# Optimization experiments

Measured on AMD Instinct MI355X. Metric: run time of the kernel, lower is better.

## Reference

```python
import jax, jax.numpy as jnp
import numpy as np

N, E, G = 10000, 320000, 256
IN_NODE, OUT_NODE, IN_EDGE, HID = 32, 32, 16, 64
BN_EPS = 1e-5


def setup_inputs() -> dict:
    key = jax.random.key(0)
    ks = jax.random.split(key, 8)
    return {
        "x": jax.random.normal(ks[0], (N, IN_NODE), jnp.float32),
        "edge_attr": jax.random.normal(ks[1], (E, IN_EDGE), jnp.float32),
        "edge_index": jax.random.randint(ks[2], (2, E), 0, N),
        "batch": jnp.sort(jax.random.randint(ks[3], (N,), 0, G)),
        "W1": jax.random.normal(ks[4], (IN_EDGE, HID), jnp.float32) * 0.1,
        "b1": jnp.zeros((HID,), jnp.float32),
        "gamma": jnp.ones((HID,), jnp.float32),
        "beta": jnp.zeros((HID,), jnp.float32),
        "W2": jax.random.normal(ks[5], (HID, IN_NODE * OUT_NODE), jnp.float32) * 0.05,
        "b2": jnp.zeros((IN_NODE * OUT_NODE,), jnp.float32),
        "W_root": jax.random.normal(ks[6], (IN_NODE, OUT_NODE), jnp.float32) * 0.1,
        "bias": jnp.zeros((OUT_NODE,), jnp.float32),
        "num_graphs": G,
    }


def reference(x, edge_attr, edge_index, batch, W1, b1, gamma, beta, W2, b2, W_root, bias, num_graphs):
    src, dst = edge_index[0], edge_index[1]
    # edge MLP: Linear -> BatchNorm1d (training-mode batch stats) -> ReLU -> Linear
    h = edge_attr @ W1 + b1                                   # [E, HID]
    mu = jnp.mean(h, axis=0)
    var = jnp.var(h, axis=0)
    h = (h - mu) * jax.lax.rsqrt(var + BN_EPS) * gamma + beta
    h = jax.nn.relu(h)
    w_e = (h @ W2 + b2).reshape(-1, x.shape[1], W_root.shape[1])  # [E, in, out]
    # gather source features, per-edge matmul, scatter-add to targets
    msgs = jnp.einsum('ei,eio->eo', x[src], w_e)              # [E, out]
    aggr = jax.ops.segment_sum(msgs, dst, num_segments=x.shape[0])
    out = aggr + x @ W_root + bias                            # [N, out]
    # global mean pool per graph
    pooled = jax.ops.segment_sum(out, batch, num_segments=num_graphs)
    counts = jax.ops.segment_sum(jnp.ones((x.shape[0],), x.dtype), batch, num_segments=num_graphs)
    return pooled / jnp.maximum(counts, 1.0)[:, None]
```

## Files before the change

### kernel.cpp

```cpp
#include <hip/hip_runtime.h>
#include <stdint.h>

typedef unsigned short u16;
typedef _Float16 f16x2 __attribute__((ext_vector_type(2)));
union U32F16 { uint32_t u; f16x2 h; };

__device__ __forceinline__ float bf2f(u16 v) {
    union { uint32_t u; float f; } c; c.u = ((uint32_t)v) << 16; return c.f;
}
__device__ __forceinline__ u16 f2bf(float f) {
    union { uint32_t u; float f; } c; c.f = f;
    uint32_t u = c.u;
    return (u16)((u + 0x7FFF + ((u >> 16) & 1)) >> 16);
}
__device__ __forceinline__ float loadf(const void* p, size_t i, int isbf) {
    return isbf ? bf2f(((const u16*)p)[i]) : ((const float*)p)[i];
}
__device__ __forceinline__ int get_isbf(const void* gamma) {
    return ((const uint32_t*)gamma)[0] != 0x3F800000u;
}

__global__ __launch_bounds__(256) void k_moments(
    const void* __restrict__ ea, const int* __restrict__ eidx,
    float* __restrict__ mom, int* __restrict__ cntn,
    const void* __restrict__ gamma, int E) {
    int isbf = get_isbf(gamma);
    __shared__ float ea_s[128][17];
    int t = threadIdx.x;
    int ii = 0, jj = 0;
    if (t >= 16 && t < 152) {
        int p = t - 16, i2 = 0;
        while (p >= 16 - i2) { p -= 16 - i2; i2++; }
        ii = i2; jj = i2 + p;
    }
    float acc = 0.f;
    int ntiles = (E + 127) >> 7;
    for (int tile = blockIdx.x; tile < ntiles; tile += gridDim.x) {
        int e0 = tile * 128;
        int cnt = min(128, E - e0);
        if (!isbf) {
            for (int u = t; u < 512; u += 256) {
                int el = u >> 2, q = u & 3;
                if (el < cnt) {
                    float4 v = *(const float4*)((const float*)ea + (size_t)(e0 + el) * 16 + q * 4);
                    ea_s[el][q * 4 + 0] = v.x; ea_s[el][q * 4 + 1] = v.y;
                    ea_s[el][q * 4 + 2] = v.z; ea_s[el][q * 4 + 3] = v.w;
                }
            }
        } else {
            int el = t >> 1, q = t & 1;
            if (el < cnt) {
                uint4 v = *(const uint4*)((const u16*)ea + (size_t)(e0 + el) * 16 + q * 8);
                const u16* h8 = (const u16*)&v;
#pragma unroll
                for (int m = 0; m < 8; m++) ea_s[el][q * 8 + m] = bf2f(h8[m]);
            }
        }
        if (t < cnt) atomicAdd(&cntn[eidx[e0 + t]], 1);
        __syncthreads();
        if (t < 16) {
            for (int e = 0; e < cnt; e++) acc += ea_s[e][t];
        } else if (t < 152) {
            for (int e = 0; e < cnt; e++) acc += ea_s[e][ii] * ea_s[e][jj];
        }
        __syncthreads();
    }
    if (t < 152) atomicAdd(&mom[t], acc);
}

__global__ __launch_bounds__(256) void k_scanprep(
    const float* __restrict__ mom,
    const void* __restrict__ W1, const void* __restrict__ b1,
    const void* __restrict__ gamma, const void* __restrict__ beta,
    const int* __restrict__ cntn, int* __restrict__ offsets,
    float* __restrict__ W1eff, float* __restrict__ b1eff, int N, float invE) {
    __shared__ float M[16][16], S[16];
    __shared__ int ssum[256];
    int t = threadIdx.x;
    int isbf = get_isbf(gamma);
    if (t < 16) S[t] = mom[t];
    if (t >= 16 && t < 152) {
        int p = t - 16, i2 = 0;
        while (p >= 16 - i2) { p -= 16 - i2; i2++; }
        float v = mom[t];
        M[i2][i2 + p] = v; M[i2 + p][i2] = v;
    }
    __syncthreads();
    if (t < 64) {
        int k = t;
        float w[16];
#pragma unroll
        for (int i = 0; i < 16; i++) w[i] = loadf(W1, (size_t)i * 64 + k, isbf);
        float s1 = 0.f;
#pragma unroll
        for (int i = 0; i < 16; i++) s1 += w[i] * S[i];
        s1 *= invE;
        float s2 = 0.f;
#pragma unroll
        for (int i = 0; i < 16; i++) {
            float r = 0.f;
#pragma unroll
            for (int j = 0; j < 16; j++) r += w[j] * M[i][j];
            s2 += w[i] * r;
        }
        s2 *= invE;
        float bk = loadf(b1, k, isbf);
        float mu = s1 + bk;
        float var = s2 - s1 * s1;
        float a = loadf(gamma, k, isbf) * rsqrtf(var + 1e-5f);
        b1eff[k] = bk * a + loadf(beta, k, isbf) - mu * a;
#pragma unroll
        for (int i = 0; i < 16; i++) W1eff[i * 64 + k] = w[i] * a;
    }
    int chunk = (N + 255) >> 8;
    int lo = min(t * chunk, N), hi = min(lo + chunk, N);
    int s = 0;
    for (int i = lo; i < hi; i++) s += cntn[i];
    ssum[t] = s; __syncthreads();
    for (int d = 1; d < 256; d <<= 1) {
        int v = (t >= d) ? ssum[t - d] : 0;
        __syncthreads();
        ssum[t] += v;
        __syncthreads();
    }
    int run = ssum[t] - s;
    for (int i = lo; i < hi; i++) { offsets[i] = run; run += cntn[i]; }
    if (t == 255) offsets[N] = run;
}

__global__ __launch_bounds__(256) void k_place(const int* __restrict__ eidx,
                                               const int* __restrict__ offsets,
                                               int* __restrict__ cursor,
                                               int* __restrict__ perm, int E) {
    int e = blockIdx.x * 256 + threadIdx.x;
    if (e < E) {
        int s = eidx[e];
        int pos = offsets[s] + atomicAdd(&cursor[s], 1);
        perm[pos] = e;
    }
}

__global__ __launch_bounds__(256) void k_nodeQ(
    const void* __restrict__ ea, const int* __restrict__ eidx,
    const void* __restrict__ x, const void* __restrict__ W2, const void* __restrict__ b2,
    const float* __restrict__ W1eff, const float* __restrict__ b1eff,
    const int* __restrict__ offsets, const int* __restrict__ perm,
    float* __restrict__ aggr, const void* __restrict__ gamma, int N, int E) {
    int n0 = blockIdx.x * 4;
    __shared__ int offs[5];
    __shared__ float xs[4][32], Rs[4][32];
    __shared__ uint32_t Qp[4][32][32];
    __shared__ float ea_s[32][16];
    __shared__ uint32_t hp[32][32];
    __shared__ int ec[32], dstc[32], sc[32];
    int t = threadIdx.x;
    if (t < 5) offs[t] = offsets[min(n0 + t, N)];
    __syncthreads();
    int off0 = offs[0], off4 = offs[4];
    if (off0 == off4) return;
    int isbf = get_isbf(gamma);

    if (t < 128) {
        int nn = t >> 5, i = t & 31;
        int n = n0 + nn;
        xs[nn][i] = (n < N) ? loadf(x, (size_t)n * 32 + i, isbf) : 0.f;
    }
    __syncthreads();
    {
        int o = t & 31, j2 = t >> 5;
        if (!isbf) {
            const float* W2f = (const float*)W2;
            for (int m = 0; m < 4; m++) {
                int jp = j2 + 8 * m;
                size_t base = (size_t)(2 * jp) * 1024 + o;
                float a[4][2];
#pragma unroll
                for (int nn = 0; nn < 4; nn++) { a[nn][0] = 0.f; a[nn][1] = 0.f; }
#pragma unroll 4
                for (int i = 0; i < 32; i++) {
                    float w0 = W2f[base + i * 32];
                    float w1 = W2f[base + 1024 + i * 32];
#pragma unroll
                    for (int nn = 0; nn < 4; nn++) {
                        float xv = xs[nn][i];
                        a[nn][0] += xv * w0; a[nn][1] += xv * w1;
                    }
                }
#pragma unroll
                for (int nn = 0; nn < 4; nn++) {
                    U32F16 p; p.h.x = (_Float16)a[nn][0]; p.h.y = (_Float16)a[nn][1];
                    Qp[nn][jp][o] = p.u;
                }
            }
        } else {
            const u16* W2h = (const u16*)W2;
            for (int m = 0; m < 4; m++) {
                int jp = j2 + 8 * m;
                size_t base = (size_t)(2 * jp) * 1024 + o;
                float a[4][2];
#pragma unroll
                for (int nn = 0; nn < 4; nn++) { a[nn][0] = 0.f; a[nn][1] = 0.f; }
#pragma unroll 4
                for (int i = 0; i < 32; i++) {
                    float w0 = bf2f(W2h[base + i * 32]);
                    float w1 = bf2f(W2h[base + 1024 + i * 32]);
#pragma unroll
                    for (int nn = 0; nn < 4; nn++) {
                        float xv = xs[nn][i];
                        a[nn][0] += xv * w0; a[nn][1] += xv * w1;
                    }
                }
#pragma unroll
                for (int nn = 0; nn < 4; nn++) {
                    U32F16 p; p.h.x = (_Float16)a[nn][0]; p.h.y = (_Float16)a[nn][1];
                    Qp[nn][jp][o] = p.u;
                }
            }
        }
    }
    if (t < 128) {
        int nn = t >> 5, o = t & 31;
        float acc = 0.f;
#pragma unroll 8
        for (int i = 0; i < 32; i++) acc += xs[nn][i] * loadf(b2, (size_t)i * 32 + o, isbf);
        Rs[nn][o] = acc;
    }
    int kk = t & 31;
    float w1a[16], w1b[16];
#pragma unroll
    for (int i = 0; i < 16; i++) {
        w1a[i] = W1eff[i * 64 + 2 * kk];
        w1b[i] = W1eff[i * 64 + 2 * kk + 1];
    }
    float bka = b1eff[2 * kk], bkb = b1eff[2 * kk + 1];

    float4 pf_f = make_float4(0, 0, 0, 0);
    uint4 pf_b = make_uint4(0, 0, 0, 0);
    int pf_e = -1, pf_me = -1, pf_dst = 0, pf_s = 0;

    auto issue = [&](int jbase) {
        pf_e = -1; pf_me = -1;
        if (!isbf) {
            if (t < 128) {
                int j = jbase + (t >> 2);
                if (j < off4) {
                    int e = perm[j];
                    pf_e = e;
                    pf_f = *(const float4*)((const float*)ea + (size_t)e * 16 + (t & 3) * 4);
                }
            }
        } else {
            if (t < 64) {
                int j = jbase + (t >> 1);
                if (j < off4) {
                    int e = perm[j];
                    pf_e = e;
                    pf_b = *(const uint4*)((const u16*)ea + (size_t)e * 16 + (t & 1) * 8);
                }
            }
        }
        if (t < 32) {
            int j = jbase + t;
            if (j < off4) {
                pf_me = perm[j];
                pf_dst = eidx[E + pf_me];
                pf_s = (j >= offs[1]) + (j >= offs[2]) + (j >= offs[3]);
            }
        }
    };

    issue(off0);
    __syncthreads();

    for (int j0 = off0; j0 < off4; j0 += 32) {
        if (!isbf) {
            if (t < 128 && pf_e >= 0) {
                int el = t >> 2, q = t & 3;
                ea_s[el][q * 4 + 0] = pf_f.x; ea_s[el][q * 4 + 1] = pf_f.y;
                ea_s[el][q * 4 + 2] = pf_f.z; ea_s[el][q * 4 + 3] = pf_f.w;
            }
        } else {
            if (t < 64 && pf_e >= 0) {
                int el = t >> 1, q = t & 1;
                const u16* h8 = (const u16*)&pf_b;
#pragma unroll
                for (int m = 0; m < 8; m++) ea_s[el][q * 8 + m] = bf2f(h8[m]);
            }
        }
        if (t < 32) { ec[t] = pf_me; dstc[t] = pf_dst; sc[t] = pf_s; }
        __syncthreads();
        issue(j0 + 32);
#pragma unroll
        for (int p = 0; p < 4; p++) {
            int e = (t >> 5) + 8 * p;
            if (ec[e] >= 0) {
                float va = bka, vb = bkb;
#pragma unroll
                for (int i = 0; i < 16; i++) {
                    float ei = ea_s[e][i];
                    va += ei * w1a[i];
                    vb += ei * w1b[i];
                }
                U32F16 ph;
                ph.h.x = (_Float16)fmaxf(va, 0.f);
                ph.h.y = (_Float16)fmaxf(vb, 0.f);
                hp[e][kk] = ph.u;
            }
        }
        __syncthreads();
#pragma unroll
        for (int p = 0; p < 4; p++) {
            int e = (t >> 5) + 8 * p;
            if (ec[e] >= 0) {
                int s = sc[e];
                f16x2 a0, a1;
                a0.x = (_Float16)0.f; a0.y = (_Float16)0.f;
                a1.x = (_Float16)0.f; a1.y = (_Float16)0.f;
#pragma unroll
                for (int j = 0; j < 32; j += 2) {
                    U32F16 qa, qb, ha, hb;
                    qa.u = Qp[s][j][kk];     ha.u = hp[e][j];
                    qb.u = Qp[s][j + 1][kk]; hb.u = hp[e][j + 1];
                    a0 += ha.h * qa.h;
                    a1 += hb.h * qb.h;
                }
                float acc = Rs[s][kk] + (float)a0.x + (float)a0.y + (float)a1.x + (float)a1.y;
                atomicAdd(&aggr[(size_t)dstc[e] * 32 + kk], acc);
            }
        }
        __syncthreads();
    }
}

__global__ __launch_bounds__(256) void k_node(
    const void* __restrict__ x, const void* __restrict__ Wr, const void* __restrict__ bias,
    const int* __restrict__ batch, const float* __restrict__ aggr,
    float* __restrict__ pooled, int* __restrict__ cntG,
    const void* __restrict__ gamma, int N) {
    int isbf = get_isbf(gamma);
    int t = threadIdx.x, o = t & 31, g = t >> 5;
    int n = blockIdx.x * 8 + g;
    if (n >= N) return;
    float acc = aggr[(size_t)n * 32 + o] + loadf(bias, o, isbf);
#pragma unroll 8
    for (int i = 0; i < 32; i++)
        acc += loadf(x, (size_t)n * 32 + i, isbf) * loadf(Wr, (size_t)i * 32 + o, isbf);
    int b = batch[n];
    atomicAdd(&pooled[(size_t)b * 32 + o], acc);
    if (o == 0) atomicAdd(&cntG[b], 1);
}

__global__ __launch_bounds__(256) void k_final(const float* __restrict__ pooled,
                                               const int* __restrict__ cntG,
                                               void* __restrict__ out,
                                               const void* __restrict__ gamma, int total) {
    int idx = blockIdx.x * 256 + threadIdx.x;
    if (idx >= total) return;
    int isbf = get_isbf(gamma);
    float c = (float)max(cntG[idx >> 5], 1);
    float v = pooled[idx] / c;
    if (isbf) ((u16*)out)[idx] = f2bf(v);
    else ((float*)out)[idx] = v;
}

extern "C" void kernel_launch(void* const* d_in, const int* in_sizes, int n_in,
                              void* d_out, int out_size, void* d_ws, size_t ws_size,
                              hipStream_t stream) {
    const void* x    = d_in[0];
    const void* ea   = d_in[1];
    const int* eidx  = (const int*)d_in[2];
    const int* batch = (const int*)d_in[3];
    const void* W1   = d_in[4];
    const void* b1   = d_in[5];
    const void* gamma= d_in[6];
    const void* beta = d_in[7];
    const void* W2   = d_in[8];
    const void* b2   = d_in[9];
    const void* Wr   = d_in[10];
    const void* bias = d_in[11];

    int N = in_sizes[0] / 32;
    int E = in_sizes[1] / 16;
    int G = out_size / 32;

    char* ws = (char*)d_ws;
    size_t off = 0;
    auto alloc = [&](size_t bytes) {
        char* p = ws + off;
        off = (off + bytes + 255) & ~(size_t)255;
        return p;
    };
    float* mom     = (float*)alloc(152 * 4);
    float* pooled  = (float*)alloc((size_t)G * 32 * 4);
    int*   cntG    = (int*)alloc((size_t)G * 4);
    float* aggr    = (float*)alloc((size_t)N * 32 * 4);
    int*   cntn    = (int*)alloc((size_t)N * 4);
    int*   cursor  = (int*)alloc((size_t)N * 4);
    size_t zero_bytes = off;
    int*   offsets = (int*)alloc((size_t)(N + 1) * 4);
    int*   perm    = (int*)alloc((size_t)E * 4);
    float* W1eff   = (float*)alloc(1024 * 4);
    float* b1eff   = (float*)alloc(64 * 4);
    (void)ws_size; (void)n_in;

    hipMemsetAsync(d_ws, 0, zero_bytes, stream);
    k_moments<<<256, 256, 0, stream>>>(ea, eidx, mom, cntn, gamma, E);
    k_scanprep<<<1, 256, 0, stream>>>(mom, W1, b1, gamma, beta, cntn, offsets,
                                      W1eff, b1eff, N, 1.0f / (float)E);
    k_place<<<(E + 255) / 256, 256, 0, stream>>>(eidx, offsets, cursor, perm, E);
    k_nodeQ<<<(N + 3) / 4, 256, 0, stream>>>(ea, eidx, x, W2, b2, W1eff, b1eff,
                                             offsets, perm, aggr, gamma, N, E);
    k_node<<<(N + 7) / 8, 256, 0, stream>>>(x, Wr, bias, batch, aggr, pooled, cntG,
                                            gamma, N);
    k_final<<<(G * 32 + 255) / 256, 256, 0, stream>>>(pooled, cntG, d_out, gamma, G * 32);
}
```

Before: 272.6 us.

## Group edges by destination and contract through W2 once per node

Edges are now bucketed by destination instead of source. Each block gathers the source x rows and builds a per-node outer-product accumulator T = sum over edges of h ⊗ x_src. It then multiplies T by W2 once with fdot2, in place of applying per-source Q matrices to every edge. The per-node aggr buffer and the k_node pass go away: the root linear term and bias are applied in k_final after pooling x by graph, using linearity. W2 is reloaded by every block and T is stored as fp16, which costs extra memory traffic and some precision.

```diff
diff --git a/kernel.cpp b/kernel.cpp
--- a/kernel.cpp
+++ b/kernel.cpp
@@ -4,6 +4,7 @@
 typedef unsigned short u16;
 typedef _Float16 f16x2 __attribute__((ext_vector_type(2)));
 union U32F16 { uint32_t u; f16x2 h; };
+union V4 { uint4 u; float4 f; };
 
 __device__ __forceinline__ float bf2f(u16 v) {
     union { uint32_t u; float f; } c; c.u = ((uint32_t)v) << 16; return c.f;
@@ -18,6 +19,20 @@
 }
 __device__ __forceinline__ int get_isbf(const void* gamma) {
     return ((const uint32_t*)gamma)[0] != 0x3F800000u;
+}
+
+#if defined(__has_builtin)
+#if __has_builtin(__builtin_amdgcn_fdot2)
+#define HAS_FDOT2 1
+#endif
+#endif
+__device__ __forceinline__ float fdot2acc(uint32_t a, uint32_t b, float c) {
+    U32F16 ua, ub; ua.u = a; ub.u = b;
+#ifdef HAS_FDOT2
+    return __builtin_amdgcn_fdot2(ua.h, ub.h, c, false);
+#else
+    return c + (float)ua.h.x * (float)ub.h.x + (float)ua.h.y * (float)ub.h.y;
+#endif
 }
 
 __global__ __launch_bounds__(256) void k_moments(
@@ -56,7 +71,7 @@
                 for (int m = 0; m < 8; m++) ea_s[el][q * 8 + m] = bf2f(h8[m]);
             }
         }
-        if (t < cnt) atomicAdd(&cntn[eidx[e0 + t]], 1);
+        if (t < cnt) atomicAdd(&cntn[eidx[E + e0 + t]], 1);
         __syncthreads();
         if (t < 16) {
             for (int e = 0; e < cnt; e++) acc += ea_s[e][t];
@@ -128,143 +143,110 @@
     if (t == 255) offsets[N] = run;
 }
 
-__global__ __launch_bounds__(256) void k_place(const int* __restrict__ eidx,
-                                               const int* __restrict__ offsets,
-                                               int* __restrict__ cursor,
-                                               int* __restrict__ perm, int E) {
-    int e = blockIdx.x * 256 + threadIdx.x;
-    if (e < E) {
-        int s = eidx[e];
-        int pos = offsets[s] + atomicAdd(&cursor[s], 1);
-        perm[pos] = e;
-    }
-}
-
-__global__ __launch_bounds__(256) void k_nodeQ(
+__global__ __launch_bounds__(256) void k_place(
+    const int* __restrict__ eidx, const int* __restrict__ offsets,
+    int* __restrict__ cursor, int* __restrict__ perm,
+    const void* __restrict__ x, const int* __restrict__ batch,
+    float* __restrict__ pooledX, int* __restrict__ cntG,
+    const void* __restrict__ gamma, int E, int N) {
+    int idx = blockIdx.x * 256 + threadIdx.x;
+    if (idx < E) {
+        int d = eidx[E + idx];
+        int pos = offsets[d] + atomicAdd(&cursor[d], 1);
+        perm[pos] = idx;
+    }
+    if (idx < N * 32) {
+        int isbf = get_isbf(gamma);
+        int n = idx >> 5, o = idx & 31;
+        int b = batch[n];
+        atomicAdd(&pooledX[(size_t)b * 32 + o], loadf(x, idx, isbf));
+        if (o == 0) atomicAdd(&cntG[b], 1);
+    }
+}
+
+__global__ __launch_bounds__(256) void k_aggrT(
     const void* __restrict__ ea, const int* __restrict__ eidx,
     const void* __restrict__ x, const void* __restrict__ W2, const void* __restrict__ b2,
     const float* __restrict__ W1eff, const float* __restrict__ b1eff,
     const int* __restrict__ offsets, const int* __restrict__ perm,
-    float* __restrict__ aggr, const void* __restrict__ gamma, int N, int E) {
+    const int* __restrict__ batch, float* __restrict__ pooledA,
+    const void* __restrict__ gamma, int N, int E) {
+    __shared__ uint32_t smem[8320];
+    float* W1s = (float*)smem;
+    float* b1s = (float*)(smem + 1024);
+    float* eas = (float*)(smem + 1088);
+    float* xss = (float*)(smem + 1600);
+    float* hss = (float*)(smem + 2624);
+    int* ecs   = (int*)(smem + 4672);
+    int* scs   = (int*)(smem + 4704);
+    int* offsS = (int*)(smem + 4736);
+    uint32_t* Ts  = smem;
+    uint32_t* W2s = smem + 4096;
+    float* XSs = (float*)(smem + 8192);
+
+    int t = threadIdx.x;
     int n0 = blockIdx.x * 4;
-    __shared__ int offs[5];
-    __shared__ float xs[4][32], Rs[4][32];
-    __shared__ uint32_t Qp[4][32][32];
-    __shared__ float ea_s[32][16];
-    __shared__ uint32_t hp[32][32];
-    __shared__ int ec[32], dstc[32], sc[32];
-    int t = threadIdx.x;
-    if (t < 5) offs[t] = offsets[min(n0 + t, N)];
+    if (t < 5) offsS[t] = offsets[min(n0 + t, N)];
     __syncthreads();
-    int off0 = offs[0], off4 = offs[4];
+    int off0 = offsS[0], o1 = offsS[1], o2 = offsS[2], o3 = offsS[3], off4 = offsS[4];
     if (off0 == off4) return;
     int isbf = get_isbf(gamma);
 
-    if (t < 128) {
-        int nn = t >> 5, i = t & 31;
-        int n = n0 + nn;
-        xs[nn][i] = (n < N) ? loadf(x, (size_t)n * 32 + i, isbf) : 0.f;
-    }
-    __syncthreads();
-    {
-        int o = t & 31, j2 = t >> 5;
-        if (!isbf) {
-            const float* W2f = (const float*)W2;
-            for (int m = 0; m < 4; m++) {
-                int jp = j2 + 8 * m;
-                size_t base = (size_t)(2 * jp) * 1024 + o;
-                float a[4][2];
-#pragma unroll
-                for (int nn = 0; nn < 4; nn++) { a[nn][0] = 0.f; a[nn][1] = 0.f; }
-#pragma unroll 4
-                for (int i = 0; i < 32; i++) {
-                    float w0 = W2f[base + i * 32];
-                    float w1 = W2f[base + 1024 + i * 32];
-#pragma unroll
-                    for (int nn = 0; nn < 4; nn++) {
-                        float xv = xs[nn][i];
-                        a[nn][0] += xv * w0; a[nn][1] += xv * w1;
-                    }
-                }
-#pragma unroll
-                for (int nn = 0; nn < 4; nn++) {
-                    U32F16 p; p.h.x = (_Float16)a[nn][0]; p.h.y = (_Float16)a[nn][1];
-                    Qp[nn][jp][o] = p.u;
-                }
-            }
-        } else {
-            const u16* W2h = (const u16*)W2;
-            for (int m = 0; m < 4; m++) {
-                int jp = j2 + 8 * m;
-                size_t base = (size_t)(2 * jp) * 1024 + o;
-                float a[4][2];
-#pragma unroll
-                for (int nn = 0; nn < 4; nn++) { a[nn][0] = 0.f; a[nn][1] = 0.f; }
-#pragma unroll 4
-                for (int i = 0; i < 32; i++) {
-                    float w0 = bf2f(W2h[base + i * 32]);
-                    float w1 = bf2f(W2h[base + 1024 + i * 32]);
-#pragma unroll
-                    for (int nn = 0; nn < 4; nn++) {
-                        float xv = xs[nn][i];
-                        a[nn][0] += xv * w0; a[nn][1] += xv * w1;
-                    }
-                }
-#pragma unroll
-                for (int nn = 0; nn < 4; nn++) {
-                    U32F16 p; p.h.x = (_Float16)a[nn][0]; p.h.y = (_Float16)a[nn][1];
-                    Qp[nn][jp][o] = p.u;
-                }
-            }
-        }
-    }
-    if (t < 128) {
-        int nn = t >> 5, o = t & 31;
-        float acc = 0.f;
-#pragma unroll 8
-        for (int i = 0; i < 32; i++) acc += xs[nn][i] * loadf(b2, (size_t)i * 32 + o, isbf);
-        Rs[nn][o] = acc;
-    }
-    int kk = t & 31;
-    float w1a[16], w1b[16];
-#pragma unroll
-    for (int i = 0; i < 16; i++) {
-        w1a[i] = W1eff[i * 64 + 2 * kk];
-        w1b[i] = W1eff[i * 64 + 2 * kk + 1];
-    }
-    float bka = b1eff[2 * kk], bkb = b1eff[2 * kk + 1];
-
-    float4 pf_f = make_float4(0, 0, 0, 0);
-    uint4 pf_b = make_uint4(0, 0, 0, 0);
-    int pf_e = -1, pf_me = -1, pf_dst = 0, pf_s = 0;
-
-    auto issue = [&](int jbase) {
-        pf_e = -1; pf_me = -1;
+    for (int i = t; i < 1024; i += 256) W1s[i] = W1eff[i];
+    if (t < 64) b1s[t] = b1eff[t];
+    float T[4][8];
+    float XS[4][4];
+#pragma unroll
+    for (int c = 0; c < 4; c++) {
+#pragma unroll
+        for (int m = 0; m < 8; m++) T[c][m] = 0.f;
+#pragma unroll
+        for (int m = 0; m < 4; m++) XS[c][m] = 0.f;
+    }
+    int kp = t & 31, iq = t >> 5;
+
+    V4 pf_ea, pf_x;
+    pf_ea.u = make_uint4(0, 0, 0, 0); pf_x.u = make_uint4(0, 0, 0, 0);
+    int pf_je = -1, pf_jx = -1, pf_me = -1, pf_ms = 0;
+
+    auto issue = [&](int jb) {
+        pf_je = -1; pf_jx = -1; pf_me = -1;
         if (!isbf) {
             if (t < 128) {
-                int j = jbase + (t >> 2);
+                int j = jb + (t >> 2);
                 if (j < off4) {
-                    int e = perm[j];
-                    pf_e = e;
-                    pf_f = *(const float4*)((const float*)ea + (size_t)e * 16 + (t & 3) * 4);
+                    int e = perm[j]; pf_je = 1;
+                    pf_ea.u = ((const uint4*)((const float*)ea + (size_t)e * 16))[t & 3];
+                }
+            }
+            {
+                int j = jb + (t >> 3);
+                if (j < off4) {
+                    int e = perm[j]; int src = eidx[e]; pf_jx = 1;
+                    pf_x.u = ((const uint4*)((const float*)x + (size_t)src * 32))[t & 7];
                 }
             }
         } else {
             if (t < 64) {
-                int j = jbase + (t >> 1);
+                int j = jb + (t >> 1);
                 if (j < off4) {
-                    int e = perm[j];
-                    pf_e = e;
-                    pf_b = *(const uint4*)((const u16*)ea + (size_t)e * 16 + (t & 1) * 8);
+                    int e = perm[j]; pf_je = 1;
+                    pf_ea.u = ((const uint4*)((const u16*)ea + (size_t)e * 16))[t & 1];
+                }
+            }
+            if (t < 128) {
+                int j = jb + (t >> 2);
+                if (j < off4) {
+                    int e = perm[j]; int src = eidx[e]; pf_jx = 1;
+                    pf_x.u = ((const uint4*)((const u16*)x + (size_t)src * 32))[t & 3];
                 }
             }
         }
         if (t < 32) {
-            int j = jbase + t;
+            int j = jb + t;
             if (j < off4) {
                 pf_me = perm[j];
-                pf_dst = eidx[E + pf_me];
-                pf_s = (j >= offs[1]) + (j >= offs[2]) + (j >= offs[3]);
+                pf_ms = (j >= o1) + (j >= o2) + (j >= o3);
             }
         }
     };
@@ -274,91 +256,152 @@
 
     for (int j0 = off0; j0 < off4; j0 += 32) {
         if (!isbf) {
-            if (t < 128 && pf_e >= 0) {
+            if (pf_je >= 0) {
                 int el = t >> 2, q = t & 3;
-                ea_s[el][q * 4 + 0] = pf_f.x; ea_s[el][q * 4 + 1] = pf_f.y;
-                ea_s[el][q * 4 + 2] = pf_f.z; ea_s[el][q * 4 + 3] = pf_f.w;
+                eas[el * 16 + q * 4 + 0] = pf_ea.f.x; eas[el * 16 + q * 4 + 1] = pf_ea.f.y;
+                eas[el * 16 + q * 4 + 2] = pf_ea.f.z; eas[el * 16 + q * 4 + 3] = pf_ea.f.w;
+            }
+            if (pf_jx >= 0) {
+                int el = t >> 3, q = t & 7;
+                xss[el * 32 + q * 4 + 0] = pf_x.f.x; xss[el * 32 + q * 4 + 1] = pf_x.f.y;
+                xss[el * 32 + q * 4 + 2] = pf_x.f.z; xss[el * 32 + q * 4 + 3] = pf_x.f.w;
             }
         } else {
-            if (t < 64 && pf_e >= 0) {
+            if (pf_je >= 0) {
                 int el = t >> 1, q = t & 1;
-                const u16* h8 = (const u16*)&pf_b;
-#pragma unroll
-                for (int m = 0; m < 8; m++) ea_s[el][q * 8 + m] = bf2f(h8[m]);
-            }
-        }
-        if (t < 32) { ec[t] = pf_me; dstc[t] = pf_dst; sc[t] = pf_s; }
+                const u16* h8 = (const u16*)&pf_ea.u;
+#pragma unroll
+                for (int m = 0; m < 8; m++) eas[el * 16 + q * 8 + m] = bf2f(h8[m]);
+            }
+            if (pf_jx >= 0) {
+                int el = t >> 2, q = t & 3;
+                const u16* h8 = (const u16*)&pf_x.u;
+#pragma unroll
+                for (int m = 0; m < 8; m++) xss[el * 32 + q * 8 + m] = bf2f(h8[m]);
+            }
+        }
+        if (t < 32) { ecs[t] = pf_me; scs[t] = pf_ms; }
         __syncthreads();
         issue(j0 + 32);
 #pragma unroll
         for (int p = 0; p < 4; p++) {
-            int e = (t >> 5) + 8 * p;
-            if (ec[e] >= 0) {
-                float va = bka, vb = bkb;
+            int e = iq + 8 * p;
+            if (ecs[e] >= 0) {
+                float va = b1s[2 * kp], vb = b1s[2 * kp + 1];
 #pragma unroll
                 for (int i = 0; i < 16; i++) {
-                    float ei = ea_s[e][i];
-                    va += ei * w1a[i];
-                    vb += ei * w1b[i];
-                }
-                U32F16 ph;
-                ph.h.x = (_Float16)fmaxf(va, 0.f);
-                ph.h.y = (_Float16)fmaxf(vb, 0.f);
-                hp[e][kk] = ph.u;
-            }
-        }
-        __syncthreads();
-#pragma unroll
-        for (int p = 0; p < 4; p++) {
-            int e = (t >> 5) + 8 * p;
-            if (ec[e] >= 0) {
-                int s = sc[e];
-                f16x2 a0, a1;
-                a0.x = (_Float16)0.f; a0.y = (_Float16)0.f;
-                a1.x = (_Float16)0.f; a1.y = (_Float16)0.f;
-#pragma unroll
-                for (int j = 0; j < 32; j += 2) {
-                    U32F16 qa, qb, ha, hb;
-                    qa.u = Qp[s][j][kk];     ha.u = hp[e][j];
-                    qb.u = Qp[s][j + 1][kk]; hb.u = hp[e][j + 1];
-                    a0 += ha.h * qa.h;
-                    a1 += hb.h * qb.h;
-                }
-                float acc = Rs[s][kk] + (float)a0.x + (float)a0.y + (float)a1.x + (float)a1.y;
-                atomicAdd(&aggr[(size_t)dstc[e] * 32 + kk], acc);
-            }
-        }
-        __syncthreads();
-    }
-}
-
-__global__ __launch_bounds__(256) void k_node(
-    const void* __restrict__ x, const void* __restrict__ Wr, const void* __restrict__ bias,
-    const int* __restrict__ batch, const float* __restrict__ aggr,
-    float* __restrict__ pooled, int* __restrict__ cntG,
-    const void* __restrict__ gamma, int N) {
-    int isbf = get_isbf(gamma);
-    int t = threadIdx.x, o = t & 31, g = t >> 5;
-    int n = blockIdx.x * 8 + g;
-    if (n >= N) return;
-    float acc = aggr[(size_t)n * 32 + o] + loadf(bias, o, isbf);
+                    float ei = eas[e * 16 + i];
+                    float2 w = *(const float2*)&W1s[i * 64 + 2 * kp];
+                    va += ei * w.x; vb += ei * w.y;
+                }
+                float2 hv; hv.x = fmaxf(va, 0.f); hv.y = fmaxf(vb, 0.f);
+                *(float2*)&hss[e * 64 + 2 * kp] = hv;
+            }
+        }
+        __syncthreads();
+#pragma unroll 4
+        for (int e = 0; e < 32; e++) {
+            if (ecs[e] < 0) continue;
+            int cs_ = scs[e];
+            float2 h2 = *(const float2*)&hss[e * 64 + 2 * kp];
+            float4 x4 = *(const float4*)&xss[e * 32 + 4 * iq];
+#define ACCC(c) { \
+            T[c][0] += h2.x * x4.x; T[c][1] += h2.x * x4.y; \
+            T[c][2] += h2.x * x4.z; T[c][3] += h2.x * x4.w; \
+            T[c][4] += h2.y * x4.x; T[c][5] += h2.y * x4.y; \
+            T[c][6] += h2.y * x4.z; T[c][7] += h2.y * x4.w; \
+            if (kp == 0) { XS[c][0] += x4.x; XS[c][1] += x4.y; \
+                           XS[c][2] += x4.z; XS[c][3] += x4.w; } }
+            switch (cs_) {
+                case 0: ACCC(0); break;
+                case 1: ACCC(1); break;
+                case 2: ACCC(2); break;
+                default: ACCC(3); break;
+            }
+#undef ACCC
+        }
+        __syncthreads();
+    }
+
+#pragma unroll
+    for (int c = 0; c < 4; c++) {
+#pragma unroll
+        for (int kk = 0; kk < 2; kk++) {
+#pragma unroll
+            for (int p = 0; p < 2; p++) {
+                int kpp = (2 * kp + kk) * 16 + 2 * iq + p;
+                int lg = c * 1024 + kpp;
+                int ph = lg ^ ((lg >> 5) & 31);
+                U32F16 pk;
+                pk.h.x = (_Float16)T[c][kk * 4 + 2 * p];
+                pk.h.y = (_Float16)T[c][kk * 4 + 2 * p + 1];
+                Ts[ph] = pk.u;
+            }
+        }
+    }
+    if (kp == 0) {
+#pragma unroll
+        for (int c = 0; c < 4; c++)
+#pragma unroll
+            for (int m = 0; m < 4; m++) XSs[c * 32 + 4 * iq + m] = XS[c][m];
+    }
+
+    int c = t >> 6, half = (t >> 5) & 1, o = t & 31;
+    float acc0 = 0.f, acc1 = 0.f;
+    for (int sec = 0; sec < 8; sec++) {
+        __syncthreads();
+        for (int it = 0; it < 16; it++) {
+            int idx = it * 256 + t;
+            int kl = idx >> 5, o2v = idx & 31;
+            int kpp = sec * 128 + kl;
+            int k = kpp >> 4, i2 = (kpp & 15) * 2;
+            U32F16 pw;
+            pw.h.x = (_Float16)loadf(W2, (size_t)k * 1024 + i2 * 32 + o2v, isbf);
+            pw.h.y = (_Float16)loadf(W2, (size_t)k * 1024 + (i2 + 1) * 32 + o2v, isbf);
+            W2s[idx] = pw.u;
+        }
+        __syncthreads();
+        int base = c * 1024 + sec * 128;
 #pragma unroll 8
-    for (int i = 0; i < 32; i++)
-        acc += loadf(x, (size_t)n * 32 + i, isbf) * loadf(Wr, (size_t)i * 32 + o, isbf);
-    int b = batch[n];
-    atomicAdd(&pooled[(size_t)b * 32 + o], acc);
-    if (o == 0) atomicAdd(&cntG[b], 1);
-}
-
-__global__ __launch_bounds__(256) void k_final(const float* __restrict__ pooled,
-                                               const int* __restrict__ cntG,
-                                               void* __restrict__ out,
-                                               const void* __restrict__ gamma, int total) {
+        for (int kl = half * 64; kl < half * 64 + 64; kl += 2) {
+            int lg0 = base + kl, lg1 = base + kl + 1;
+            int ph0 = lg0 ^ ((lg0 >> 5) & 31);
+            int ph1 = lg1 ^ ((lg1 >> 5) & 31);
+            acc0 = fdot2acc(Ts[ph0], W2s[kl * 32 + o], acc0);
+            acc1 = fdot2acc(Ts[ph1], W2s[(kl + 1) * 32 + o], acc1);
+        }
+    }
+    float acc = acc0 + acc1;
+    acc += __shfl_xor(acc, 32);
+    if (half == 0) {
+        float bacc = 0.f;
+#pragma unroll 8
+        for (int i = 0; i < 32; i++) bacc += XSs[c * 32 + i] * loadf(b2, (size_t)i * 32 + o, isbf);
+        acc += bacc;
+        int n = n0 + c;
+        if (n < N) {
+            int g = batch[n];
+            atomicAdd(&pooledA[(size_t)g * 32 + o], acc);
+        }
+    }
+}
+
+__global__ __launch_bounds__(256) void k_final(
+    const float* __restrict__ pooledA, const float* __restrict__ pooledX,
+    const int* __restrict__ cntG, const void* __restrict__ Wr,
+    const void* __restrict__ bias, void* __restrict__ out,
+    const void* __restrict__ gamma, int total) {
     int idx = blockIdx.x * 256 + threadIdx.x;
     if (idx >= total) return;
     int isbf = get_isbf(gamma);
-    float c = (float)max(cntG[idx >> 5], 1);
-    float v = pooled[idx] / c;
+    int g = idx >> 5, o = idx & 31;
+    float v = pooledA[idx];
+#pragma unroll 8
+    for (int i = 0; i < 32; i++)
+        v += pooledX[(size_t)g * 32 + i] * loadf(Wr, (size_t)i * 32 + o, isbf);
+    int c = cntG[g];
+    v += (float)c * loadf(bias, o, isbf);
+    v /= (float)max(c, 1);
     if (isbf) ((u16*)out)[idx] = f2bf(v);
     else ((float*)out)[idx] = v;
 }
@@ -391,9 +434,9 @@
         return p;
     };
     float* mom     = (float*)alloc(152 * 4);
-    float* pooled  = (float*)alloc((size_t)G * 32 * 4);
+    float* pooledA = (float*)alloc((size_t)G * 32 * 4);
+    float* pooledX = (float*)alloc((size_t)G * 32 * 4);
     int*   cntG    = (int*)alloc((size_t)G * 4);
-    float* aggr    = (float*)alloc((size_t)N * 32 * 4);
     int*   cntn    = (int*)alloc((size_t)N * 4);
     int*   cursor  = (int*)alloc((size_t)N * 4);
     size_t zero_bytes = off;
@@ -407,10 +450,11 @@
     k_moments<<<256, 256, 0, stream>>>(ea, eidx, mom, cntn, gamma, E);
     k_scanprep<<<1, 256, 0, stream>>>(mom, W1, b1, gamma, beta, cntn, offsets,
                                       W1eff, b1eff, N, 1.0f / (float)E);
-    k_place<<<(E + 255) / 256, 256, 0, stream>>>(eidx, offsets, cursor, perm, E);
-    k_nodeQ<<<(N + 3) / 4, 256, 0, stream>>>(ea, eidx, x, W2, b2, W1eff, b1eff,
-                                             offsets, perm, aggr, gamma, N, E);
-    k_node<<<(N + 7) / 8, 256, 0, stream>>>(x, Wr, bias, batch, aggr, pooled, cntG,
-                                            gamma, N);
-    k_final<<<(G * 32 + 255) / 256, 256, 0, stream>>>(pooled, cntG, d_out, gamma, G * 32);
-}
+    int pl_total = max(E, N * 32);
+    k_place<<<(pl_total + 255) / 256, 256, 0, stream>>>(eidx, offsets, cursor, perm,
+                                                        x, batch, pooledX, cntG, gamma, E, N);
+    k_aggrT<<<(N + 3) / 4, 256, 0, stream>>>(ea, eidx, x, W2, b2, W1eff, b1eff,
+                                             offsets, perm, batch, pooledA, gamma, N, E);
+    k_final<<<(G * 32 + 255) / 256, 256, 0, stream>>>(pooledA, pooledX, cntG, Wr, bias,
+                                                      d_out, gamma, G * 32);
+}
```

Result: slower. 668.2 us (+145.2%).

## Pool messages directly per graph and fold root term into final kernel

Applied to the files above, without the earlier changes.

Edge messages are now atomically added straight into per-graph pooled sums, sharded eight ways, instead of a per-node aggregate buffer, which removes the aggr array and the k_node pass. The root linear term becomes linear in pooled x: x is pooled per graph in k_place and multiplied by W_root once per graph in k_final. The edge loop is restructured so each 64-lane wave handles one source node, two edges per iteration, with Q kept in registers, fdot2 accumulation and waitcnt instead of block barriers. The costs are more atomics onto a small pooled array (eased by sharding), relying on wave-local LDS ordering without barriers, and lower parallelism per edge.

```diff
diff --git a/kernel.cpp b/kernel.cpp
--- a/kernel.cpp
+++ b/kernel.cpp
@@ -19,6 +19,21 @@
 __device__ __forceinline__ int get_isbf(const void* gamma) {
     return ((const uint32_t*)gamma)[0] != 0x3F800000u;
 }
+
+#if defined(__has_builtin)
+#if __has_builtin(__builtin_amdgcn_fdot2)
+#define HAS_FDOT2 1
+#endif
+#endif
+__device__ __forceinline__ float fdot2acc(uint32_t a, uint32_t b, float c) {
+    U32F16 ua, ub; ua.u = a; ub.u = b;
+#ifdef HAS_FDOT2
+    return __builtin_amdgcn_fdot2(ua.h, ub.h, c, false);
+#else
+    return c + (float)ua.h.x * (float)ub.h.x + (float)ua.h.y * (float)ub.h.y;
+#endif
+}
+#define LGKM_WAIT() __asm__ volatile("s_waitcnt lgkmcnt(0)" ::: "memory")
 
 __global__ __launch_bounds__(256) void k_moments(
     const void* __restrict__ ea, const int* __restrict__ eidx,
@@ -128,44 +143,52 @@
     if (t == 255) offsets[N] = run;
 }
 
-__global__ __launch_bounds__(256) void k_place(const int* __restrict__ eidx,
-                                               const int* __restrict__ offsets,
-                                               int* __restrict__ cursor,
-                                               int* __restrict__ perm, int E) {
-    int e = blockIdx.x * 256 + threadIdx.x;
-    if (e < E) {
-        int s = eidx[e];
+__global__ __launch_bounds__(256) void k_place(
+    const int* __restrict__ eidx, const int* __restrict__ offsets,
+    int* __restrict__ cursor, int* __restrict__ perm,
+    const void* __restrict__ x, const int* __restrict__ batch,
+    float* __restrict__ pooledX8, int* __restrict__ cntG8,
+    const void* __restrict__ gamma, int E, int N, int G) {
+    int idx = blockIdx.x * 256 + threadIdx.x;
+    int shard = blockIdx.x & 7;
+    if (idx < E) {
+        int s = eidx[idx];
         int pos = offsets[s] + atomicAdd(&cursor[s], 1);
-        perm[pos] = e;
-    }
-}
-
-__global__ __launch_bounds__(256) void k_nodeQ(
+        perm[pos] = idx;
+    }
+    if (idx < N * 32) {
+        int isbf = get_isbf(gamma);
+        int n = idx >> 5, o = idx & 31;
+        int b = batch[n];
+        atomicAdd(&pooledX8[((size_t)shard * G + b) * 32 + o], loadf(x, idx, isbf));
+        if (o == 0) atomicAdd(&cntG8[shard * G + b], 1);
+    }
+}
+
+__global__ __launch_bounds__(256, 4) void k_nodeQ(
     const void* __restrict__ ea, const int* __restrict__ eidx,
     const void* __restrict__ x, const void* __restrict__ W2, const void* __restrict__ b2,
     const float* __restrict__ W1eff, const float* __restrict__ b1eff,
     const int* __restrict__ offsets, const int* __restrict__ perm,
-    float* __restrict__ aggr, const void* __restrict__ gamma, int N, int E) {
-    int n0 = blockIdx.x * 4;
+    const int* __restrict__ batch, float* __restrict__ pooledA8,
+    const void* __restrict__ gamma, int N, int E, int G) {
     __shared__ int offs[5];
     __shared__ float xs[4][32], Rs[4][32];
     __shared__ uint32_t Qp[4][32][32];
-    __shared__ float ea_s[32][16];
-    __shared__ uint32_t hp[32][32];
-    __shared__ int ec[32], dstc[32], sc[32];
+    __shared__ alignas(16) float eaw[4][2][16];
+    __shared__ alignas(16) uint32_t hw[4][2][32];
     int t = threadIdx.x;
+    int n0 = blockIdx.x * 4;
     if (t < 5) offs[t] = offsets[min(n0 + t, N)];
-    __syncthreads();
-    int off0 = offs[0], off4 = offs[4];
-    if (off0 == off4) return;
     int isbf = get_isbf(gamma);
-
     if (t < 128) {
         int nn = t >> 5, i = t & 31;
         int n = n0 + nn;
         xs[nn][i] = (n < N) ? loadf(x, (size_t)n * 32 + i, isbf) : 0.f;
     }
     __syncthreads();
+    if (offs[0] == offs[4]) return;
+
     {
         int o = t & 31, j2 = t >> 5;
         if (!isbf) {
@@ -225,142 +248,121 @@
         for (int i = 0; i < 32; i++) acc += xs[nn][i] * loadf(b2, (size_t)i * 32 + o, isbf);
         Rs[nn][o] = acc;
     }
-    int kk = t & 31;
+    __syncthreads();
+
+    int w = t >> 6, lane = t & 63, o = lane & 31, half = lane >> 5;
+    int lo = offs[w], hi = offs[w + 1];
     float w1a[16], w1b[16];
 #pragma unroll
     for (int i = 0; i < 16; i++) {
-        w1a[i] = W1eff[i * 64 + 2 * kk];
-        w1b[i] = W1eff[i * 64 + 2 * kk + 1];
-    }
-    float bka = b1eff[2 * kk], bkb = b1eff[2 * kk + 1];
-
-    float4 pf_f = make_float4(0, 0, 0, 0);
-    uint4 pf_b = make_uint4(0, 0, 0, 0);
-    int pf_e = -1, pf_me = -1, pf_dst = 0, pf_s = 0;
-
-    auto issue = [&](int jbase) {
-        pf_e = -1; pf_me = -1;
+        w1a[i] = W1eff[i * 64 + 2 * o];
+        w1b[i] = W1eff[i * 64 + 2 * o + 1];
+    }
+    float bka = b1eff[2 * o], bkb = b1eff[2 * o + 1];
+    uint32_t qreg[32];
+#pragma unroll
+    for (int j = 0; j < 32; j++) qreg[j] = Qp[w][j][o];
+    float Rv = Rs[w][o];
+    float* poolbase = pooledA8 + (size_t)(blockIdx.x & 7) * G * 32;
+
+    for (int j0 = lo; j0 < hi; j0 += 2) {
+        int jme = j0 + half;
+        int e = -1, g = 0;
+        if (jme < hi) {
+            e = perm[jme];
+            g = batch[eidx[E + e]];
+        }
         if (!isbf) {
-            if (t < 128) {
-                int j = jbase + (t >> 2);
-                if (j < off4) {
-                    int e = perm[j];
-                    pf_e = e;
-                    pf_f = *(const float4*)((const float*)ea + (size_t)e * 16 + (t & 3) * 4);
+            if (lane < 8) {
+                int js = j0 + (lane >> 2);
+                if (js < hi) {
+                    int es = perm[js];
+                    *(float4*)&eaw[w][lane >> 2][(lane & 3) * 4] =
+                        *(const float4*)((const float*)ea + (size_t)es * 16 + (lane & 3) * 4);
                 }
             }
         } else {
-            if (t < 64) {
-                int j = jbase + (t >> 1);
-                if (j < off4) {
-                    int e = perm[j];
-                    pf_e = e;
-                    pf_b = *(const uint4*)((const u16*)ea + (size_t)e * 16 + (t & 1) * 8);
-                }
-            }
-        }
-        if (t < 32) {
-            int j = jbase + t;
-            if (j < off4) {
-                pf_me = perm[j];
-                pf_dst = eidx[E + pf_me];
-                pf_s = (j >= offs[1]) + (j >= offs[2]) + (j >= offs[3]);
-            }
-        }
-    };
-
-    issue(off0);
+            if (lane < 4) {
+                int js = j0 + (lane >> 1);
+                if (js < hi) {
+                    int es = perm[js];
+                    uint4 v = *(const uint4*)((const u16*)ea + (size_t)es * 16 + (lane & 1) * 8);
+                    const u16* h8 = (const u16*)&v;
+                    float4 f0 = make_float4(bf2f(h8[0]), bf2f(h8[1]), bf2f(h8[2]), bf2f(h8[3]));
+                    float4 f1 = make_float4(bf2f(h8[4]), bf2f(h8[5]), bf2f(h8[6]), bf2f(h8[7]));
+                    *(float4*)&eaw[w][lane >> 1][(lane & 1) * 8] = f0;
+                    *(float4*)&eaw[w][lane >> 1][(lane & 1) * 8 + 4] = f1;
+                }
+            }
+        }
+        LGKM_WAIT();
+        if (e >= 0) {
+            const float4* eq = (const float4*)&eaw[w][half][0];
+            float4 e0 = eq[0], e1 = eq[1], e2 = eq[2], e3 = eq[3];
+            float ee[16];
+            *(float4*)&ee[0] = e0; *(float4*)&ee[4] = e1;
+            *(float4*)&ee[8] = e2; *(float4*)&ee[12] = e3;
+            float va = bka, vb = bkb;
+#pragma unroll
+            for (int i = 0; i < 16; i++) { va += ee[i] * w1a[i]; vb += ee[i] * w1b[i]; }
+            U32F16 ph;
+            ph.h.x = (_Float16)fmaxf(va, 0.f);
+            ph.h.y = (_Float16)fmaxf(vb, 0.f);
+            hw[w][half][o] = ph.u;
+        }
+        LGKM_WAIT();
+        if (e >= 0) {
+            float acc = Rv;
+            const uint4* hq = (const uint4*)&hw[w][half][0];
+#pragma unroll
+            for (int j4 = 0; j4 < 8; j4++) {
+                uint4 hv = hq[j4];
+                acc = fdot2acc(hv.x, qreg[4 * j4 + 0], acc);
+                acc = fdot2acc(hv.y, qreg[4 * j4 + 1], acc);
+                acc = fdot2acc(hv.z, qreg[4 * j4 + 2], acc);
+                acc = fdot2acc(hv.w, qreg[4 * j4 + 3], acc);
+            }
+            atomicAdd(poolbase + (size_t)g * 32 + o, acc);
+        }
+    }
+}
+
+__global__ __launch_bounds__(256) void k_final(
+    const float* __restrict__ pooledA8, const float* __restrict__ pooledX8,
+    const int* __restrict__ cntG8, const void* __restrict__ Wr,
+    const void* __restrict__ bias, void* __restrict__ out,
+    const void* __restrict__ gamma, int G) {
+    __shared__ float px[8][32];
+    __shared__ int cg[8];
+    int t = threadIdx.x;
+    int g0 = blockIdx.x * 8;
+    int gg = t >> 5, o = t & 31;
+    int g = g0 + gg;
+    int isbf = get_isbf(gamma);
+    if (g < G) {
+        float s = 0.f;
+#pragma unroll
+        for (int sh = 0; sh < 8; sh++) s += pooledX8[((size_t)sh * G + g) * 32 + o];
+        px[gg][o] = s;
+        if (o == 0) {
+            int c = 0;
+#pragma unroll
+            for (int sh = 0; sh < 8; sh++) c += cntG8[sh * G + g];
+            cg[gg] = c;
+        }
+    }
     __syncthreads();
-
-    for (int j0 = off0; j0 < off4; j0 += 32) {
-        if (!isbf) {
-            if (t < 128 && pf_e >= 0) {
-                int el = t >> 2, q = t & 3;
-                ea_s[el][q * 4 + 0] = pf_f.x; ea_s[el][q * 4 + 1] = pf_f.y;
-                ea_s[el][q * 4 + 2] = pf_f.z; ea_s[el][q * 4 + 3] = pf_f.w;
-            }
-        } else {
-            if (t < 64 && pf_e >= 0) {
-                int el = t >> 1, q = t & 1;
-                const u16* h8 = (const u16*)&pf_b;
-#pragma unroll
-                for (int m = 0; m < 8; m++) ea_s[el][q * 8 + m] = bf2f(h8[m]);
-            }
-        }
-        if (t < 32) { ec[t] = pf_me; dstc[t] = pf_dst; sc[t] = pf_s; }
-        __syncthreads();
-        issue(j0 + 32);
-#pragma unroll
-        for (int p = 0; p < 4; p++) {
-            int e = (t >> 5) + 8 * p;
-            if (ec[e] >= 0) {
-                float va = bka, vb = bkb;
-#pragma unroll
-                for (int i = 0; i < 16; i++) {
-                    float ei = ea_s[e][i];
-                    va += ei * w1a[i];
-                    vb += ei * w1b[i];
-                }
-                U32F16 ph;
-                ph.h.x = (_Float16)fmaxf(va, 0.f);
-                ph.h.y = (_Float16)fmaxf(vb, 0.f);
-                hp[e][kk] = ph.u;
-            }
-        }
-        __syncthreads();
-#pragma unroll
-        for (int p = 0; p < 4; p++) {
-            int e = (t >> 5) + 8 * p;
-            if (ec[e] >= 0) {
-                int s = sc[e];
-                f16x2 a0, a1;
-                a0.x = (_Float16)0.f; a0.y = (_Float16)0.f;
-                a1.x = (_Float16)0.f; a1.y = (_Float16)0.f;
-#pragma unroll
-                for (int j = 0; j < 32; j += 2) {
-                    U32F16 qa, qb, ha, hb;
-                    qa.u = Qp[s][j][kk];     ha.u = hp[e][j];
-                    qb.u = Qp[s][j + 1][kk]; hb.u = hp[e][j + 1];
-                    a0 += ha.h * qa.h;
-                    a1 += hb.h * qb.h;
-                }
-                float acc = Rs[s][kk] + (float)a0.x + (float)a0.y + (float)a1.x + (float)a1.y;
-                atomicAdd(&aggr[(size_t)dstc[e] * 32 + kk], acc);
-            }
-        }
-        __syncthreads();
-    }
-}
-
-__global__ __launch_bounds__(256) void k_node(
-    const void* __restrict__ x, const void* __restrict__ Wr, const void* __restrict__ bias,
-    const int* __restrict__ batch, const float* __restrict__ aggr,
-    float* __restrict__ pooled, int* __restrict__ cntG,
-    const void* __restrict__ gamma, int N) {
-    int isbf = get_isbf(gamma);
-    int t = threadIdx.x, o = t & 31, g = t >> 5;
-    int n = blockIdx.x * 8 + g;
-    if (n >= N) return;
-    float acc = aggr[(size_t)n * 32 + o] + loadf(bias, o, isbf);
+    if (g >= G) return;
+    float v = 0.f;
+#pragma unroll
+    for (int sh = 0; sh < 8; sh++) v += pooledA8[((size_t)sh * G + g) * 32 + o];
 #pragma unroll 8
-    for (int i = 0; i < 32; i++)
-        acc += loadf(x, (size_t)n * 32 + i, isbf) * loadf(Wr, (size_t)i * 32 + o, isbf);
-    int b = batch[n];
-    atomicAdd(&pooled[(size_t)b * 32 + o], acc);
-    if (o == 0) atomicAdd(&cntG[b], 1);
-}
-
-__global__ __launch_bounds__(256) void k_final(const float* __restrict__ pooled,
-                                               const int* __restrict__ cntG,
-                                               void* __restrict__ out,
-                                               const void* __restrict__ gamma, int total) {
-    int idx = blockIdx.x * 256 + threadIdx.x;
-    if (idx >= total) return;
-    int isbf = get_isbf(gamma);
-    float c = (float)max(cntG[idx >> 5], 1);
-    float v = pooled[idx] / c;
-    if (isbf) ((u16*)out)[idx] = f2bf(v);
-    else ((float*)out)[idx] = v;
+    for (int i = 0; i < 32; i++) v += px[gg][i] * loadf(Wr, (size_t)i * 32 + o, isbf);
+    int c = cg[gg];
+    v += (float)c * loadf(bias, o, isbf);
+    v /= (float)max(c, 1);
+    if (isbf) ((u16*)out)[g * 32 + o] = f2bf(v);
+    else ((float*)out)[g * 32 + o] = v;
 }
 
 extern "C" void kernel_launch(void* const* d_in, const int* in_sizes, int n_in,
@@ -390,27 +392,30 @@
         off = (off + bytes + 255) & ~(size_t)255;
         return p;
     };
-    float* mom     = (float*)alloc(152 * 4);
-    float* pooled  = (float*)alloc((size_t)G * 32 * 4);
-    int*   cntG    = (int*)alloc((size_t)G * 4);
-    float* aggr    = (float*)alloc((size_t)N * 32 * 4);
-    int*   cntn    = (int*)alloc((size_t)N * 4);
-    int*   cursor  = (int*)alloc((size_t)N * 4);
+    float* mom      = (float*)alloc(152 * 4);
+    float* pooledA8 = (float*)alloc((size_t)8 * G * 32 * 4);
+    float* pooledX8 = (float*)alloc((size_t)8 * G * 32 * 4);
+    int*   cntG8    = (int*)alloc((size_t)8 * G * 4);
+    int*   cntn     = (int*)alloc((size_t)N * 4);
+    int*   cursor   = (int*)alloc((size_t)N * 4);
     size_t zero_bytes = off;
-    int*   offsets = (int*)alloc((size_t)(N + 1) * 4);
-    int*   perm    = (int*)alloc((size_t)E * 4);
-    float* W1eff   = (float*)alloc(1024 * 4);
-    float* b1eff   = (float*)alloc(64 * 4);
+    int*   offsets  = (int*)alloc((size_t)(N + 1) * 4);
+    int*   perm     = (int*)alloc((size_t)E * 4);
+    float* W1eff    = (float*)alloc(1024 * 4);
+    float* b1eff    = (float*)alloc(64 * 4);
     (void)ws_size; (void)n_in;
 
     hipMemsetAsync(d_ws, 0, zero_bytes, stream);
     k_moments<<<256, 256, 0, stream>>>(ea, eidx, mom, cntn, gamma, E);
     k_scanprep<<<1, 256, 0, stream>>>(mom, W1, b1, gamma, beta, cntn, offsets,
                                       W1eff, b1eff, N, 1.0f / (float)E);
-    k_place<<<(E + 255) / 256, 256, 0, stream>>>(eidx, offsets, cursor, perm, E);
+    int pl_total = max(E, N * 32);
+    k_place<<<(pl_total + 255) / 256, 256, 0, stream>>>(eidx, offsets, cursor, perm,
+                                                        x, batch, pooledX8, cntG8,
+                                                        gamma, E, N, G);
     k_nodeQ<<<(N + 3) / 4, 256, 0, stream>>>(ea, eidx, x, W2, b2, W1eff, b1eff,
-                                             offsets, perm, aggr, gamma, N, E);
-    k_node<<<(N + 7) / 8, 256, 0, stream>>>(x, Wr, bias, batch, aggr, pooled, cntG,
-                                            gamma, N);
-    k_final<<<(G * 32 + 255) / 256, 256, 0, stream>>>(pooled, cntG, d_out, gamma, G * 32);
-}
+                                             offsets, perm, batch, pooledA8,
+                                             gamma, N, E, G);
+    k_final<<<(G + 7) / 8, 256, 0, stream>>>(pooledA8, pooledX8, cntG8, Wr, bias,
+                                             d_out, gamma, G);
+}
```

New measurement: 321.6 us. 1.18x slower.
